# Kernel tuning notes

Measured on AMD Instinct MI355X. Metric: run time of the kernel, lower is better.

The kernel has to match this reference:

```python
import jax, jax.numpy as jnp
import numpy as np

DIM, WIDTH = 5, 64
BATCH, N_SAVE = 4096, 64
RTOL, ATOL = 1e-3, 1e-6
SAFETY, FMIN, FMAX = 0.9, 0.2, 10.0
MAX_STEPS, DT0, EPS = 64, 0.1, 1e-6

# Tsit5 (Tsitouras 2011) Butcher tableau
A21 = 0.161
A31, A32 = -0.008480655492356989, 0.335480655492357
A41, A42, A43 = 2.8971530571054935, -6.359448489975075, 4.3622954328695815
A51, A52, A53, A54 = 5.325864828439257, -11.748883564062828, 7.4955393428898365, -0.09249506636175525
A61, A62, A63, A64, A65 = 5.86145544294642, -12.92096931784711, 8.159367898576159, -0.071584973281401, -0.028269050394068383
B1, B2, B3, B4, B5, B6 = 0.09646076681806523, 0.01, 0.4798896504144996, 1.379008574103742, -3.290069515436081, 2.324710524099774
# embedded 4th-order error coefficients (b - bhat)
E1, E2, E3, E4, E5, E6, E7 = (-0.00178001105222577714, -0.0008164344596567469,
    0.007880878010261995, -0.1447110071732629, 0.5823571654525552,
    -0.45808210592918697, 0.015151515151515152)


def _mlp(y, W1, b1, W2, b2, W3, b3, W4, b4):
    # eqx.nn.MLP(5, 5, width 64, depth 3, softplus)
    h = jax.nn.softplus(y @ W1.T + b1)
    h = jax.nn.softplus(h @ W2.T + b2)
    h = jax.nn.softplus(h @ W3.T + b3)
    return h @ W4.T + b4


def _solve_one(y0, t_eval, params):
    f = lambda y: _mlp(y, *params)
    t0, t1 = t_eval[0], t_eval[-1]
    # save points at/before t0 get y0
    ys0 = jnp.where((t_eval <= t0 + EPS)[:, None], y0[None, :], 0.0)

    def body(carry, _):
        t, y, h, ys = carry
        done = t >= t1 - EPS
        hc = jnp.where(done, 0.0, jnp.minimum(h, t1 - t))  # clip last step to t1
        k1 = f(y)
        k2 = f(y + hc * (A21 * k1))
        k3 = f(y + hc * (A31 * k1 + A32 * k2))
        k4 = f(y + hc * (A41 * k1 + A42 * k2 + A43 * k3))
        k5 = f(y + hc * (A51 * k1 + A52 * k2 + A53 * k3 + A54 * k4))
        k6 = f(y + hc * (A61 * k1 + A62 * k2 + A63 * k3 + A64 * k4 + A65 * k5))
        ynew = y + hc * (B1 * k1 + B2 * k2 + B3 * k3 + B4 * k4 + B5 * k5 + B6 * k6)
        k7 = f(ynew)  # FSAL stage, also used for error + interpolation
        err = hc * (E1 * k1 + E2 * k2 + E3 * k3 + E4 * k4 + E5 * k5 + E6 * k6 + E7 * k7)
        scale = ATOL + RTOL * jnp.maximum(jnp.abs(y), jnp.abs(ynew))
        enorm = jnp.sqrt(jnp.mean((err / scale) ** 2))
        enorm_c = jax.lax.stop_gradient(jnp.maximum(enorm, 1e-10))
        accept = enorm <= 1.0
        factor = jnp.clip(SAFETY * enorm_c ** -0.2, FMIN, FMAX)  # I-controller, order 5
        step_ok = accept & ~done
        t_next = jnp.where(step_ok, t + hc, t)
        y_next = jnp.where(step_ok, ynew, y)
        h_next = jnp.where(done, h, hc * factor)
        # cubic Hermite interpolation for save points inside (t, t_next]
        s = ((t_eval - t) / jnp.maximum(hc, 1e-12))[:, None]
        h00 = 2 * s**3 - 3 * s**2 + 1
        h10 = s**3 - 2 * s**2 + s
        h01 = -2 * s**3 + 3 * s**2
        h11 = s**3 - s**2
        yi = h00 * y + h10 * hc * k1 + h01 * ynew + h11 * hc * k7
        mask = (t_eval > t) & (t_eval <= t_next + EPS) & step_ok
        ys = jnp.where(mask[:, None], yi, ys)
        return (t_next, y_next, h_next, ys), None

    h0 = jnp.asarray(DT0, dtype=y0.dtype)
    (_, _, _, ys), _ = jax.lax.scan(body, (t0, y0, h0, ys0), None, length=MAX_STEPS)
    return ys  # [N_SAVE, DIM]


def setup_inputs() -> dict:
    key = jax.random.key(0)
    ks = jax.random.split(key, 9)
    y0 = jax.random.normal(ks[0], (BATCH, DIM), dtype=jnp.float32)
    t_eval = jnp.linspace(0.0, 1.0, N_SAVE, dtype=jnp.float32)

    def lin(k, out_d, in_d):
        lim = 1.0 / np.sqrt(in_d)
        kw, kb = jax.random.split(k)
        W = jax.random.uniform(kw, (out_d, in_d), jnp.float32, -lim, lim)
        b = jax.random.uniform(kb, (out_d,), jnp.float32, -lim, lim)
        return W, b

    W1, b1 = lin(ks[1], WIDTH, DIM)
    W2, b2 = lin(ks[2], WIDTH, WIDTH)
    W3, b3 = lin(ks[3], WIDTH, WIDTH)
    W4, b4 = lin(ks[4], DIM, WIDTH)
    return {"y0": y0, "t_eval": t_eval, "W1": W1, "b1": b1, "W2": W2, "b2": b2,
            "W3": W3, "b3": b3, "W4": W4, "b4": b4}


def reference(y0, t_eval, W1, b1, W2, b2, W3, b3, W4, b4):
    params = (W1, b1, W2, b2, W3, b3, W4, b4)
    return jax.vmap(lambda y: _solve_one(y, t_eval, params))(y0)  # [BATCH, N_SAVE, DIM]
```

## Files before the change

kernel.cpp:

```cpp
#include <hip/hip_runtime.h>
#include <cmath>

namespace {

constexpr int kDim = 5;
constexpr int kSave = 64;
constexpr int kTraj = 16;
constexpr int kThreads = 256;
constexpr int kMaxSteps = 64;
constexpr int HS = 72;
constexpr int SD = 8;
constexpr int OS = kTraj * kDim;

typedef _Float16 half8 __attribute__((ext_vector_type(8)));
typedef float f32x4 __attribute__((ext_vector_type(4)));

__device__ __forceinline__ float softplusf(float x) {
  return fmaxf(x, 0.0f) + __logf(1.0f + __expf(-fabsf(x)));
}

__device__ __forceinline__ void barrier_lgkm() {
  asm volatile("s_waitcnt lgkmcnt(0)" ::: "memory");
  __builtin_amdgcn_s_barrier();
  asm volatile("" ::: "memory");
}

struct FragsA { half8 h0a, h1a, l0a, l1a; };

__global__ __launch_bounds__(kThreads, 1)
void node_tsit5_kernel(const float* __restrict__ gy0,
                       const float* __restrict__ gte,
                       const float* __restrict__ gW1, const float* __restrict__ gb1,
                       const float* __restrict__ gW2, const float* __restrict__ gb2,
                       const float* __restrict__ gW3, const float* __restrict__ gb3,
                       const float* __restrict__ gW4, const float* __restrict__ gb4,
                       float* __restrict__ out) {
  const float A21 = 0.161f;
  const float A31 = -0.008480655492356989f, A32 = 0.335480655492357f;
  const float A41 = 2.8971530571054935f, A42 = -6.359448489975075f, A43 = 4.3622954328695815f;
  const float A51 = 5.325864828439257f, A52 = -11.748883564062828f, A53 = 7.4955393428898365f,
              A54 = -0.09249506636175525f;
  const float A61 = 5.86145544294642f, A62 = -12.92096931784711f, A63 = 8.159367898576159f,
              A64 = -0.071584973281401f, A65 = -0.028269050394068383f;
  const float B1 = 0.09646076681806523f, B2 = 0.01f, B3 = 0.4798896504144996f,
              B4 = 1.379008574103742f, B5 = -3.290069515436081f, B6 = 2.324710524099774f;
  const float E1 = -0.00178001105222577714f, E2 = -0.0008164344596567469f,
              E3 = 0.007880878010261995f, E4 = -0.1447110071732629f, E5 = 0.5823571654525552f,
              E6 = -0.45808210592918697f, E7 = 0.015151515151515152f;

  __shared__ __align__(16) _Float16 h0[kTraj * HS], l0[kTraj * HS];
  __shared__ __align__(16) _Float16 h1[kTraj * HS], l1[kTraj * HS];
  __shared__ __align__(16) _Float16 h2[kTraj * HS], l2[kTraj * HS];
  __shared__ float sTe[kSave];
  __shared__ float sY[kTraj * SD], sYN[kTraj * SD], sK1[kTraj * SD], sK7[kTraj * SD];
  __shared__ float ctT[kTraj], ctH[kTraj], ctN[kTraj], ctO[kTraj];
  __shared__ __align__(16) float sOut[kSave * OS];

  const int tid = threadIdx.x;
  const int bid = blockIdx.x;
  const int w = tid >> 6;
  const int ln = tid & 63;
  const int quad = ln >> 4;
  const int col = ln & 15;
  const int row0 = quad * 4;
  const int nn = (w << 4) | col;
  const bool cact = col < kDim;
  const bool w0 = (w == 0);

  half8 w2h[2], w3h[2], w4h[2], mfh[2];
  float w1r[kDim];
  #pragma unroll
  for (int d = 0; d < kDim; ++d) w1r[d] = gW1[nn * 5 + d];
  #pragma unroll
  for (int kf = 0; kf < 2; ++kf)
    #pragma unroll
    for (int j = 0; j < 8; ++j) {
      int kk2 = kf * 32 + quad * 8 + j;
      w2h[kf][j] = (_Float16)gW2[nn * 64 + kk2];
      w3h[kf][j] = (_Float16)gW3[nn * 64 + kk2];
      w4h[kf][j] = cact ? (_Float16)gW4[col * 64 + kk2] : (_Float16)0.0f;
      float m = 0.0f;
      #pragma unroll
      for (int d = 0; d < kDim; ++d) m = fmaf(w1r[d], gW4[d * 64 + kk2], m);
      mfh[kf][j] = (_Float16)m;
    }
  const float c1 = gb1[nn], c2 = gb2[nn], c3 = gb3[nn];
  const float c4 = cact ? gb4[col] : 0.0f;
  float cu = 0.0f;
  #pragma unroll
  for (int d = 0; d < kDim; ++d) cu = fmaf(w1r[d], gb4[d], cu);

  if (tid < kSave) sTe[tid] = gte[tid];
  if (tid < kTraj * kDim) {
    int t = tid & 15, d = tid >> 4;
    sY[t * SD + d] = gy0[(size_t)(bid * kTraj + t) * kDim + d];
  }
  {
    f32x4 zz = {0.f, 0.f, 0.f, 0.f};
    f32x4* z4 = (f32x4*)sOut;
    for (int i = tid; i < (kSave * OS) / 4; i += kThreads) z4[i] = zz;
  }

  f32x4 syr = {0, 0, 0, 0}, synr = {0, 0, 0, 0}, kk[7], uu[7], p_y;
  #pragma unroll
  for (int r = 0; r < 4; ++r) {
    const float* yr = gy0 + (size_t)(bid * kTraj + row0 + r) * kDim;
    float acc = c1;
    #pragma unroll
    for (int d = 0; d < kDim; ++d) acc = fmaf(w1r[d], yr[d], acc);
    p_y[r] = acc;
    if (cact) syr[r] = yr[col];
  }
  barrier_lgkm();

  const float t0v = sTe[0];
  const float t1v = sTe[kSave - 1];

  {
    int tt = tid & 15, gg = tid >> 4;
    float yv[kDim];
    #pragma unroll
    for (int d = 0; d < kDim; ++d) yv[d] = sY[tt * SD + d];
    #pragma unroll
    for (int q = 0; q < 4; ++q) {
      int n = 4 * gg + q;
      if (sTe[n] <= t0v + 1e-6f) {
        float* op = sOut + n * OS + tt * kDim;
        #pragma unroll
        for (int d = 0; d < kDim; ++d) op[d] = yv[d];
      }
    }
  }

  auto stageA = [&](f32x4 pre1) {
    #pragma unroll
    for (int r = 0; r < 4; ++r) {
      float s = softplusf(pre1[r]);
      _Float16 hi = (_Float16)s;
      h0[(row0 + r) * HS + nn] = hi;
      l0[(row0 + r) * HS + nn] = (_Float16)(s - (float)hi);
    }
  };

  auto loadA0 = [&]() {
    FragsA f;
    f.h0a = *(const half8*)(h0 + col * HS + quad * 8);
    f.h1a = *(const half8*)(h0 + col * HS + 32 + quad * 8);
    f.l0a = *(const half8*)(l0 + col * HS + quad * 8);
    f.l1a = *(const half8*)(l0 + col * HS + 32 + quad * 8);
    return f;
  };

  auto evalR = [&](FragsA f, f32x4& kOut, f32x4& uOut) {
    {
      f32x4 a = {c2, c2, c2, c2};
      f32x4 b = {0, 0, 0, 0};
      a = __builtin_amdgcn_mfma_f32_16x16x32_f16(f.h0a, w2h[0], a, 0, 0, 0);
      b = __builtin_amdgcn_mfma_f32_16x16x32_f16(f.l0a, w2h[0], b, 0, 0, 0);
      a = __builtin_amdgcn_mfma_f32_16x16x32_f16(f.h1a, w2h[1], a, 0, 0, 0);
      b = __builtin_amdgcn_mfma_f32_16x16x32_f16(f.l1a, w2h[1], b, 0, 0, 0);
      a += b;
      #pragma unroll
      for (int r = 0; r < 4; ++r) {
        float s = softplusf(a[r]);
        _Float16 hi = (_Float16)s;
        h1[(row0 + r) * HS + nn] = hi;
        l1[(row0 + r) * HS + nn] = (_Float16)(s - (float)hi);
      }
    }
    barrier_lgkm();
    {
      half8 ah0 = *(const half8*)(h1 + col * HS + quad * 8);
      half8 ah1 = *(const half8*)(h1 + col * HS + 32 + quad * 8);
      half8 al0 = *(const half8*)(l1 + col * HS + quad * 8);
      half8 al1 = *(const half8*)(l1 + col * HS + 32 + quad * 8);
      f32x4 a = {c3, c3, c3, c3};
      f32x4 b = {0, 0, 0, 0};
      a = __builtin_amdgcn_mfma_f32_16x16x32_f16(ah0, w3h[0], a, 0, 0, 0);
      b = __builtin_amdgcn_mfma_f32_16x16x32_f16(al0, w3h[0], b, 0, 0, 0);
      a = __builtin_amdgcn_mfma_f32_16x16x32_f16(ah1, w3h[1], a, 0, 0, 0);
      b = __builtin_amdgcn_mfma_f32_16x16x32_f16(al1, w3h[1], b, 0, 0, 0);
      a += b;
      #pragma unroll
      for (int r = 0; r < 4; ++r) {
        float s = softplusf(a[r]);
        _Float16 hi = (_Float16)s;
        h2[(row0 + r) * HS + nn] = hi;
        l2[(row0 + r) * HS + nn] = (_Float16)(s - (float)hi);
      }
    }
    barrier_lgkm();
    {
      half8 ah0 = *(const half8*)(h2 + col * HS + quad * 8);
      half8 ah1 = *(const half8*)(h2 + col * HS + 32 + quad * 8);
      half8 al0 = *(const half8*)(l2 + col * HS + quad * 8);
      half8 al1 = *(const half8*)(l2 + col * HS + 32 + quad * 8);
      f32x4 ka = {c4, c4, c4, c4};
      f32x4 kb = {0, 0, 0, 0};
      f32x4 ua = {cu, cu, cu, cu};
      f32x4 ub = {0, 0, 0, 0};
      ka = __builtin_amdgcn_mfma_f32_16x16x32_f16(ah0, w4h[0], ka, 0, 0, 0);
      kb = __builtin_amdgcn_mfma_f32_16x16x32_f16(al0, w4h[0], kb, 0, 0, 0);
      ua = __builtin_amdgcn_mfma_f32_16x16x32_f16(ah0, mfh[0], ua, 0, 0, 0);
      ub = __builtin_amdgcn_mfma_f32_16x16x32_f16(al0, mfh[0], ub, 0, 0, 0);
      ka = __builtin_amdgcn_mfma_f32_16x16x32_f16(ah1, w4h[1], ka, 0, 0, 0);
      kb = __builtin_amdgcn_mfma_f32_16x16x32_f16(al1, w4h[1], kb, 0, 0, 0);
      ua = __builtin_amdgcn_mfma_f32_16x16x32_f16(ah1, mfh[1], ua, 0, 0, 0);
      ub = __builtin_amdgcn_mfma_f32_16x16x32_f16(al1, mfh[1], ub, 0, 0, 0);
      kOut = ka + kb;
      uOut = ua + ub;
    }
  };

  stageA(p_y);
  barrier_lgkm();
  evalR(loadA0(), kk[0], uu[0]);

  f32x4 tcur = {t0v, t0v, t0v, t0v};
  f32x4 hcur = {0.1f, 0.1f, 0.1f, 0.1f};
  f32x4 hcs, tOldr;
  bool dnr[4];
  bool alldone;

  auto head = [&]() {
    bool all4 = true;
    #pragma unroll
    for (int r = 0; r < 4; ++r) {
      bool d = tcur[r] >= t1v - 1e-6f;
      dnr[r] = d;
      all4 &= d;
      hcs[r] = d ? 0.0f : fminf(hcur[r], t1v - tcur[r]);
      tOldr[r] = tcur[r];
    }
    alldone = (__ballot(all4) == ~0ull);
  };

  head();
  if (!alldone) {
    f32x4 p1;
    #pragma unroll
    for (int r = 0; r < 4; ++r) p1[r] = fmaf(hcs[r], A21 * uu[0][r], p_y[r]);
    stageA(p1);
  }
  barrier_lgkm();
  FragsA fNext = loadA0();

  for (int step = 0; step < kMaxSteps && !alldone; ++step) {
    f32x4 p1;
    evalR(fNext, kk[1], uu[1]);

    #pragma unroll
    for (int r = 0; r < 4; ++r)
      p1[r] = fmaf(hcs[r], fmaf(A32, uu[1][r], A31 * uu[0][r]), p_y[r]);
    stageA(p1); barrier_lgkm(); evalR(loadA0(), kk[2], uu[2]);

    #pragma unroll
    for (int r = 0; r < 4; ++r)
      p1[r] = fmaf(hcs[r], fmaf(A43, uu[2][r], fmaf(A42, uu[1][r], A41 * uu[0][r])), p_y[r]);
    stageA(p1); barrier_lgkm(); evalR(loadA0(), kk[3], uu[3]);

    #pragma unroll
    for (int r = 0; r < 4; ++r)
      p1[r] = fmaf(hcs[r], fmaf(A54, uu[3][r], fmaf(A53, uu[2][r],
                  fmaf(A52, uu[1][r], A51 * uu[0][r]))), p_y[r]);
    stageA(p1); barrier_lgkm(); evalR(loadA0(), kk[4], uu[4]);

    #pragma unroll
    for (int r = 0; r < 4; ++r)
      p1[r] = fmaf(hcs[r], fmaf(A65, uu[4][r], fmaf(A64, uu[3][r], fmaf(A63, uu[2][r],
                  fmaf(A62, uu[1][r], A61 * uu[0][r])))), p_y[r]);
    stageA(p1); barrier_lgkm(); evalR(loadA0(), kk[5], uu[5]);

    f32x4 bu;
    #pragma unroll
    for (int r = 0; r < 4; ++r) {
      bu[r] = fmaf(B6, uu[5][r], fmaf(B5, uu[4][r], fmaf(B4, uu[3][r],
              fmaf(B3, uu[2][r], fmaf(B2, uu[1][r], B1 * uu[0][r])))));
      synr[r] = fmaf(hcs[r], fmaf(B6, kk[5][r], fmaf(B5, kk[4][r], fmaf(B4, kk[3][r],
                 fmaf(B3, kk[2][r], fmaf(B2, kk[1][r], B1 * kk[0][r]))))), syr[r]);
      p1[r] = fmaf(hcs[r], bu[r], p_y[r]);
    }
    if (w0 && cact) {
      #pragma unroll
      for (int r = 0; r < 4; ++r) {
        int o = (row0 + r) * SD + col;
        sY[o] = syr[r];
        sYN[o] = synr[r];
        sK1[o] = kk[0][r];
      }
    }
    stageA(p1); barrier_lgkm(); evalR(loadA0(), kk[6], uu[6]);

    f32x4 rr2;
    #pragma unroll
    for (int r = 0; r < 4; ++r) {
      float err = hcs[r] * fmaf(E7, kk[6][r], fmaf(E6, kk[5][r], fmaf(E5, kk[4][r],
                  fmaf(E4, kk[3][r], fmaf(E3, kk[2][r], fmaf(E2, kk[1][r], E1 * kk[0][r]))))));
      float sc = fmaf(1e-3f, fmaxf(fabsf(syr[r]), fabsf(synr[r])), 1e-6f);
      float rr = err / sc;
      rr2[r] = cact ? rr * rr : 0.0f;
    }
    #pragma unroll
    for (int m = 1; m < 16; m <<= 1) {
      #pragma unroll
      for (int r = 0; r < 4; ++r) rr2[r] += __shfl_xor(rr2[r], m, 64);
    }

    bool okr[4];
    #pragma unroll
    for (int r = 0; r < 4; ++r) {
      float e2 = rr2[r] * 0.2f;
      bool accept = e2 <= 1.0f;
      float e2c = fmaxf(e2, 1e-20f);
      float factor = fminf(fmaxf(0.9f * __expf(-0.1f * __logf(e2c)), 0.2f), 10.0f);
      bool ok = accept && !dnr[r];
      okr[r] = ok;
      tcur[r] = ok ? tcur[r] + hcs[r] : tcur[r];
      hcur[r] = dnr[r] ? hcur[r] : hcs[r] * factor;
    }

    if (w0 && cact) {
      #pragma unroll
      for (int r = 0; r < 4; ++r) sK7[(row0 + r) * SD + col] = kk[6][r];
    }
    if (w0 && col == 0) {
      #pragma unroll
      for (int r = 0; r < 4; ++r) {
        int m2 = row0 + r;
        ctT[m2] = tOldr[r];
        ctH[m2] = hcs[r];
        ctN[m2] = tcur[r];
        ctO[m2] = okr[r] ? 1.0f : 0.0f;
      }
    }

    #pragma unroll
    for (int r = 0; r < 4; ++r) {
      if (okr[r]) {
        syr[r] = synr[r];
        kk[0][r] = kk[6][r];
        uu[0][r] = uu[6][r];
        p_y[r] = fmaf(hcs[r], bu[r], p_y[r]);
      }
    }

    head();
    if (!alldone) {
      f32x4 pn;
      #pragma unroll
      for (int r = 0; r < 4; ++r) pn[r] = fmaf(hcs[r], A21 * uu[0][r], p_y[r]);
      stageA(pn);
    }
    __attribute__((unused)) int dummy = 0;
    barrier_lgkm();

    fNext = loadA0();

    {
      int tt = tid & 15, gg = tid >> 4;
      if (ctO[tt] != 0.0f) {
        float tOld = ctT[tt], hcv = ctH[tt], tNew = ctN[tt];
        float inv = 1.0f / fmaxf(hcv, 1e-12f);
        float yv[kDim], ynv[kDim], k1v[kDim], k7v[kDim];
        #pragma unroll
        for (int d = 0; d < kDim; ++d) {
          yv[d] = sY[tt * SD + d];
          ynv[d] = sYN[tt * SD + d];
          k1v[d] = hcv * sK1[tt * SD + d];
          k7v[d] = hcv * sK7[tt * SD + d];
        }
        #pragma unroll
        for (int q = 0; q < 4; ++q) {
          int n = 4 * gg + q;
          float te = sTe[n];
          if (te > tOld && te <= tNew + 1e-6f) {
            float sx = (te - tOld) * inv;
            float s2 = sx * sx, s3 = s2 * sx;
            float h00 = 2.f * s3 - 3.f * s2 + 1.f;
            float h10 = s3 - 2.f * s2 + sx;
            float h01 = -2.f * s3 + 3.f * s2;
            float h11 = s3 - s2;
            float* op = sOut + n * OS + tt * kDim;
            #pragma unroll
            for (int d = 0; d < kDim; ++d)
              op[d] = h00 * yv[d] + h10 * k1v[d] + h01 * ynv[d] + h11 * k7v[d];
          }
        }
      }
    }
  }

  barrier_lgkm();
  {
    float* ob = out + (size_t)bid * (kTraj * kSave * kDim);
    for (int idx = tid; idx < kTraj * kSave * kDim; idx += kThreads) {
      int traj = idx / (kSave * kDim);
      int p = idx - traj * (kSave * kDim);
      int n = p / kDim;
      int d = p - n * kDim;
      ob[idx] = sOut[n * OS + traj * kDim + d];
    }
  }
}

}

extern "C" void kernel_launch(void* const* d_in, const int* in_sizes, int n_in,
                              void* d_out, int out_size, void* d_ws, size_t ws_size,
                              hipStream_t stream) {
  const float* y0 = (const float*)d_in[0];
  const float* te = (const float*)d_in[1];
  const float* W1 = (const float*)d_in[2];
  const float* b1 = (const float*)d_in[3];
  const float* W2 = (const float*)d_in[4];
  const float* b2 = (const float*)d_in[5];
  const float* W3 = (const float*)d_in[6];
  const float* b3 = (const float*)d_in[7];
  const float* W4 = (const float*)d_in[8];
  const float* b4 = (const float*)d_in[9];
  float* out = (float*)d_out;

  const int batch = in_sizes[0] / kDim;
  const int blocks = batch / kTraj;
  hipLaunchKernelGGL(node_tsit5_kernel, dim3(blocks), dim3(kThreads), 0, stream,
                     y0, te, W1, b1, W2, b2, W3, b3, W4, b4, out);
}
```

Measured before the change: 106.3 us.

## Vectorize LDS output staging, use DPP reductions and packed fp16 conversion

Pads the shared output staging buffer to an 8-float stride per trajectory so interpolated states are written and read with 128-bit LDS accesses. Replaces the shuffle-based 16-lane error-norm reduction with DPP row operations, and uses packed round-toward-zero fp16 conversion for the hi/lo split of softplus activations. It also precomputes the error partial sum and scale before the k7-dependent part. Several micro-optimisations are bundled together. The cost is doubled staging LDS, and the fp16 rounding mode changes from round-to-nearest to round-toward-zero.

```diff
diff --git a/kernel.cpp b/kernel.cpp
--- a/kernel.cpp
+++ b/kernel.cpp
@@ -10,9 +10,10 @@
 constexpr int kMaxSteps = 64;
 constexpr int HS = 72;
 constexpr int SD = 8;
-constexpr int OS = kTraj * kDim;
+constexpr int OSS = 8;
 
 typedef _Float16 half8 __attribute__((ext_vector_type(8)));
+typedef __fp16 fp16x2 __attribute__((ext_vector_type(2)));
 typedef float f32x4 __attribute__((ext_vector_type(4)));
 
 __device__ __forceinline__ float softplusf(float x) {
@@ -23,6 +24,12 @@
   asm volatile("s_waitcnt lgkmcnt(0)" ::: "memory");
   __builtin_amdgcn_s_barrier();
   asm volatile("" ::: "memory");
+}
+
+template <int Ctrl>
+__device__ __forceinline__ float dpp_add(float v) {
+  int t = __builtin_amdgcn_update_dpp(0, __float_as_int(v), Ctrl, 0xf, 0xf, false);
+  return v + __int_as_float(t);
 }
 
 struct FragsA { half8 h0a, h1a, l0a, l1a; };
@@ -52,9 +59,10 @@
   __shared__ __align__(16) _Float16 h1[kTraj * HS], l1[kTraj * HS];
   __shared__ __align__(16) _Float16 h2[kTraj * HS], l2[kTraj * HS];
   __shared__ float sTe[kSave];
-  __shared__ float sY[kTraj * SD], sYN[kTraj * SD], sK1[kTraj * SD], sK7[kTraj * SD];
+  __shared__ __align__(16) float sY[kTraj * SD], sYN[kTraj * SD];
+  __shared__ __align__(16) float sK1[kTraj * SD], sK7[kTraj * SD];
   __shared__ float ctT[kTraj], ctH[kTraj], ctN[kTraj], ctO[kTraj];
-  __shared__ __align__(16) float sOut[kSave * OS];
+  __shared__ __align__(16) float sOut[kSave * kTraj * OSS];
 
   const int tid = threadIdx.x;
   const int bid = blockIdx.x;
@@ -98,7 +106,7 @@
   {
     f32x4 zz = {0.f, 0.f, 0.f, 0.f};
     f32x4* z4 = (f32x4*)sOut;
-    for (int i = tid; i < (kSave * OS) / 4; i += kThreads) z4[i] = zz;
+    for (int i = tid; i < (kSave * kTraj * OSS) / 4; i += kThreads) z4[i] = zz;
   }
 
   f32x4 syr = {0, 0, 0, 0}, synr = {0, 0, 0, 0}, kk[7], uu[7], p_y;
@@ -118,29 +126,34 @@
 
   {
     int tt = tid & 15, gg = tid >> 4;
-    float yv[kDim];
-    #pragma unroll
-    for (int d = 0; d < kDim; ++d) yv[d] = sY[tt * SD + d];
+    const int sb = tt * SD;
+    f32x4 yv4 = *(const f32x4*)(sY + sb);
+    float yv4e = sY[sb + 4];
     #pragma unroll
     for (int q = 0; q < 4; ++q) {
       int n = 4 * gg + q;
       if (sTe[n] <= t0v + 1e-6f) {
-        float* op = sOut + n * OS + tt * kDim;
-        #pragma unroll
-        for (int d = 0; d < kDim; ++d) op[d] = yv[d];
+        float* op = sOut + (n * kTraj + tt) * OSS;
+        *(f32x4*)op = yv4;
+        op[4] = yv4e;
       }
     }
   }
 
-  auto stageA = [&](f32x4 pre1) {
-    #pragma unroll
-    for (int r = 0; r < 4; ++r) {
-      float s = softplusf(pre1[r]);
-      _Float16 hi = (_Float16)s;
-      h0[(row0 + r) * HS + nn] = hi;
-      l0[(row0 + r) * HS + nn] = (_Float16)(s - (float)hi);
-    }
+  auto sp4 = [&](const f32x4& a, _Float16* hp, _Float16* lp) {
+    float s0 = softplusf(a[0]), s1 = softplusf(a[1]);
+    float s2 = softplusf(a[2]), s3 = softplusf(a[3]);
+    fp16x2 hA = __builtin_amdgcn_cvt_pkrtz(s0, s1);
+    fp16x2 hB = __builtin_amdgcn_cvt_pkrtz(s2, s3);
+    fp16x2 lA = __builtin_amdgcn_cvt_pkrtz(s0 - (float)hA[0], s1 - (float)hA[1]);
+    fp16x2 lB = __builtin_amdgcn_cvt_pkrtz(s2 - (float)hB[0], s3 - (float)hB[1]);
+    hp[(row0 + 0) * HS + nn] = (_Float16)hA[0]; lp[(row0 + 0) * HS + nn] = (_Float16)lA[0];
+    hp[(row0 + 1) * HS + nn] = (_Float16)hA[1]; lp[(row0 + 1) * HS + nn] = (_Float16)lA[1];
+    hp[(row0 + 2) * HS + nn] = (_Float16)hB[0]; lp[(row0 + 2) * HS + nn] = (_Float16)lB[0];
+    hp[(row0 + 3) * HS + nn] = (_Float16)hB[1]; lp[(row0 + 3) * HS + nn] = (_Float16)lB[1];
   };
+
+  auto stageA = [&](const f32x4& pre1) { sp4(pre1, h0, l0); };
 
   auto loadA0 = [&]() {
     FragsA f;
@@ -160,13 +173,7 @@
       a = __builtin_amdgcn_mfma_f32_16x16x32_f16(f.h1a, w2h[1], a, 0, 0, 0);
       b = __builtin_amdgcn_mfma_f32_16x16x32_f16(f.l1a, w2h[1], b, 0, 0, 0);
       a += b;
-      #pragma unroll
-      for (int r = 0; r < 4; ++r) {
-        float s = softplusf(a[r]);
-        _Float16 hi = (_Float16)s;
-        h1[(row0 + r) * HS + nn] = hi;
-        l1[(row0 + r) * HS + nn] = (_Float16)(s - (float)hi);
-      }
+      sp4(a, h1, l1);
     }
     barrier_lgkm();
     {
@@ -181,13 +188,7 @@
       a = __builtin_amdgcn_mfma_f32_16x16x32_f16(ah1, w3h[1], a, 0, 0, 0);
       b = __builtin_amdgcn_mfma_f32_16x16x32_f16(al1, w3h[1], b, 0, 0, 0);
       a += b;
-      #pragma unroll
-      for (int r = 0; r < 4; ++r) {
-        float s = softplusf(a[r]);
-        _Float16 hi = (_Float16)s;
-        h2[(row0 + r) * HS + nn] = hi;
-        l2[(row0 + r) * HS + nn] = (_Float16)(s - (float)hi);
-      }
+      sp4(a, h2, l2);
     }
     barrier_lgkm();
     {
@@ -280,6 +281,13 @@
                  fmaf(B3, kk[2][r], fmaf(B2, kk[1][r], B1 * kk[0][r]))))), syr[r]);
       p1[r] = fmaf(hcs[r], bu[r], p_y[r]);
     }
+    f32x4 epart, scv;
+    #pragma unroll
+    for (int r = 0; r < 4; ++r) {
+      epart[r] = fmaf(E6, kk[5][r], fmaf(E5, kk[4][r], fmaf(E4, kk[3][r],
+                 fmaf(E3, kk[2][r], fmaf(E2, kk[1][r], E1 * kk[0][r])))));
+      scv[r] = fmaf(1e-3f, fmaxf(fabsf(syr[r]), fabsf(synr[r])), 1e-6f);
+    }
     if (w0 && cact) {
       #pragma unroll
       for (int r = 0; r < 4; ++r) {
@@ -294,16 +302,18 @@
     f32x4 rr2;
     #pragma unroll
     for (int r = 0; r < 4; ++r) {
-      float err = hcs[r] * fmaf(E7, kk[6][r], fmaf(E6, kk[5][r], fmaf(E5, kk[4][r],
-                  fmaf(E4, kk[3][r], fmaf(E3, kk[2][r], fmaf(E2, kk[1][r], E1 * kk[0][r]))))));
-      float sc = fmaf(1e-3f, fmaxf(fabsf(syr[r]), fabsf(synr[r])), 1e-6f);
-      float rr = err / sc;
+      float err = hcs[r] * fmaf(E7, kk[6][r], epart[r]);
+      float rr = err / scv[r];
       rr2[r] = cact ? rr * rr : 0.0f;
     }
     #pragma unroll
-    for (int m = 1; m < 16; m <<= 1) {
-      #pragma unroll
-      for (int r = 0; r < 4; ++r) rr2[r] += __shfl_xor(rr2[r], m, 64);
+    for (int r = 0; r < 4; ++r) {
+      float v = rr2[r];
+      v = dpp_add<0xB1>(v);
+      v = dpp_add<0x4E>(v);
+      v = dpp_add<0x124>(v);
+      v = dpp_add<0x128>(v);
+      rr2[r] = v;
     }
 
     bool okr[4];
@@ -351,7 +361,6 @@
       for (int r = 0; r < 4; ++r) pn[r] = fmaf(hcs[r], A21 * uu[0][r], p_y[r]);
       stageA(pn);
     }
-    __attribute__((unused)) int dummy = 0;
     barrier_lgkm();
 
     fNext = loadA0();
@@ -361,14 +370,13 @@
       if (ctO[tt] != 0.0f) {
         float tOld = ctT[tt], hcv = ctH[tt], tNew = ctN[tt];
         float inv = 1.0f / fmaxf(hcv, 1e-12f);
-        float yv[kDim], ynv[kDim], k1v[kDim], k7v[kDim];
-        #pragma unroll
-        for (int d = 0; d < kDim; ++d) {
-          yv[d] = sY[tt * SD + d];
-          ynv[d] = sYN[tt * SD + d];
-          k1v[d] = hcv * sK1[tt * SD + d];
-          k7v[d] = hcv * sK7[tt * SD + d];
-        }
+        const int sb = tt * SD;
+        f32x4 y4  = *(const f32x4*)(sY  + sb); float y4e  = sY [sb + 4];
+        f32x4 yn4 = *(const f32x4*)(sYN + sb); float yn4e = sYN[sb + 4];
+        f32x4 k14 = *(const f32x4*)(sK1 + sb); float k14e = sK1[sb + 4];
+        f32x4 k74 = *(const f32x4*)(sK7 + sb); float k74e = sK7[sb + 4];
+        k14 *= hcv; k14e *= hcv;
+        k74 *= hcv; k74e *= hcv;
         #pragma unroll
         for (int q = 0; q < 4; ++q) {
           int n = 4 * gg + q;
@@ -380,10 +388,11 @@
             float h10 = s3 - 2.f * s2 + sx;
             float h01 = -2.f * s3 + 3.f * s2;
             float h11 = s3 - s2;
-            float* op = sOut + n * OS + tt * kDim;
-            #pragma unroll
-            for (int d = 0; d < kDim; ++d)
-              op[d] = h00 * yv[d] + h10 * k1v[d] + h01 * ynv[d] + h11 * k7v[d];
+            f32x4 o = h00 * y4 + h10 * k14 + h01 * yn4 + h11 * k74;
+            float oe = h00 * y4e + h10 * k14e + h01 * yn4e + h11 * k74e;
+            float* op = sOut + (n * kTraj + tt) * OSS;
+            *(f32x4*)op = o;
+            op[4] = oe;
           }
         }
       }
@@ -398,7 +407,7 @@
       int p = idx - traj * (kSave * kDim);
       int n = p / kDim;
       int d = p - n * kDim;
-      ob[idx] = sOut[n * OS + traj * kDim + d];
+      ob[idx] = sOut[(n * kTraj + traj) * OSS + d];
     }
   }
 }
```

New measurement: 105.6 us. About the same (-0.7%).
